# Kernel tuning notes

Measured on AMD Instinct MI355X. Metric: run time of the kernel, lower is better.

## Reference

```python
import jax, jax.numpy as jnp
import numpy as np

UNITS = 256
FEAT = 256
NUM_BLOCKS = 4  # start_gru + 2 middle blocks + end_gru
BATCH, T = 128, 384


def _gru_layer(x, kernel, rkernel, bias, return_sequences):
    """Keras GRU (reset_after=True, tanh/sigmoid), zero initial state.
    x: [B,T,D]; kernel: [D,3U]; rkernel: [U,3U]; bias: [2,3U] (input, recurrent).
    Gate order z, r, h as in Keras.
    """
    u = rkernel.shape[0]
    # Precompute input projections for all timesteps (one big GEMM)
    xp = jnp.einsum('btd,dg->btg', x, kernel) + bias[0]  # [B,T,3U]

    def step(h, xt):
        rh = h @ rkernel + bias[1]                 # [B,3U]
        mz, mr, mh = jnp.split(xt, 3, axis=-1)
        rz, rr, rhh = jnp.split(rh, 3, axis=-1)
        z = jax.nn.sigmoid(mz + rz)
        r = jax.nn.sigmoid(mr + rr)
        hh = jnp.tanh(mh + r * rhh)                # reset_after: r applied after recurrent matmul
        h_new = z * h + (1.0 - z) * hh
        return h_new, h_new

    h0 = jnp.zeros((x.shape[0], u), dtype=x.dtype)
    hT, hs = jax.lax.scan(step, h0, jnp.swapaxes(xp, 0, 1))  # scan over time
    return jnp.swapaxes(hs, 0, 1) if return_sequences else hT


def setup_inputs() -> dict:
    key = jax.random.key(0)
    ks = jax.random.split(key, 8)
    s_in = 1.0 / np.sqrt(FEAT)
    s_u = 1.0 / np.sqrt(UNITS)
    x = jax.random.normal(ks[0], (BATCH, T, FEAT), dtype=jnp.float32)
    # first layer params
    k0 = jax.random.normal(ks[1], (FEAT, 3 * UNITS), dtype=jnp.float32) * s_in
    rk0 = jax.random.normal(ks[2], (UNITS, 3 * UNITS), dtype=jnp.float32) * s_u
    b0 = jnp.zeros((2, 3 * UNITS), dtype=jnp.float32)
    # remaining NUM_BLOCKS-1 layers, stacked along leading axis
    L = NUM_BLOCKS - 1
    kern = jax.random.normal(ks[3], (L, UNITS, 3 * UNITS), dtype=jnp.float32) * s_u
    rkern = jax.random.normal(ks[4], (L, UNITS, 3 * UNITS), dtype=jnp.float32) * s_u
    bias = jnp.zeros((L, 2, 3 * UNITS), dtype=jnp.float32)
    return {"x": x, "k0": k0, "rk0": rk0, "b0": b0,
            "kern": kern, "rkern": rkern, "bias": bias}


def reference(x, k0, rk0, b0, kern, rkern, bias):
    # start_gru: return_sequences=True
    h = _gru_layer(x, k0, rk0, b0, return_sequences=True)
    L = kern.shape[0]
    # middle blocks return_sequences=True, last (end_gru) returns final state only
    for i in range(L):
        last = (i == L - 1)
        h = _gru_layer(h, kern[i], rkern[i], bias[i], return_sequences=not last)
    return h  # [B, UNITS]
```

## Files before the change

kernel.cpp:

```cpp
#include <hip/hip_runtime.h>
#include <hip/hip_fp16.h>


#define LAYERS 4
#define TSTEPS 384
#define NCH    8
#define WPL    (48 * 16 * 64 * 8)
#define TILE_STRIDE (16 * 64 * 8)
#define RING   16
#define SLOT_ULL (16 * 128)
#define GRP_ULL  (RING * SLOT_ULL)

typedef _Float16 half8 __attribute__((ext_vector_type(8)));
typedef float    f32x4 __attribute__((ext_vector_type(4)));
typedef unsigned uint4v __attribute__((ext_vector_type(4)));
typedef unsigned long long ull;

#define WP_OFF   0
#define BP_OFF   (LAYERS * WPL * 2)
#define FLAG_OFF (BP_OFF + LAYERS * 1024 * 4)
#define FLAG_BYTES 4096
#define HBUF_OFF (4 * 1024 * 1024)

#define SCOPE __HIP_MEMORY_SCOPE_AGENT
#define MFMA __builtin_amdgcn_mfma_f32_16x16x32_f16

__global__ void repack_kernel(const float* __restrict__ k0, const float* __restrict__ rk0,
                              const float* __restrict__ b0, const float* __restrict__ kern,
                              const float* __restrict__ rkern, const float* __restrict__ bias,
                              _Float16* __restrict__ Wp, float* __restrict__ Bp)
{
    int idx = blockIdx.x * 256 + threadIdx.x;
    const int total_w = LAYERS * WPL;
    if (idx < total_w) {
        int l = idx / WPL;
        int r = idx - l * WPL;
        int j    = r & 7;
        int lane = (r >> 3) & 63;
        int kt   = (r >> 9) & 15;
        int tile = r >> 13;
        int n = tile * 16 + (lane & 15);
        int k = kt * 32 + (lane >> 4) * 8 + j;
        float v;
        if (l == 0) {
            v = (k < 256) ? k0[(size_t)k * 768 + n] : rk0[(size_t)(k - 256) * 768 + n];
        } else {
            const float* kk = kern  + (size_t)(l - 1) * 256 * 768;
            const float* rk = rkern + (size_t)(l - 1) * 256 * 768;
            v = (k < 256) ? kk[(size_t)k * 768 + n] : rk[(size_t)(k - 256) * 768 + n];
        }
        Wp[idx] = (_Float16)v;
    } else {
        int ib = idx - total_w;
        if (ib < LAYERS * 1024) {
            int l = ib >> 10;
            int i = ib & 1023;
            const float* bs = (l == 0) ? b0 : (bias + (size_t)(l - 1) * 2 * 768);
            float v;
            if (i < 512)      v = bs[i] + bs[768 + i];
            else if (i < 768) v = bs[512 + (i - 512)];
            else              v = bs[768 + 512 + (i - 768)];
            Bp[l * 1024 + i] = v;
        }
    }
}

__launch_bounds__(512, 2)
__global__ void gru_kernel(const float* __restrict__ x,
                           const _Float16* __restrict__ Wp,
                           const float* __restrict__ Bp,
                           ull* __restrict__ hbuf,
                           unsigned int* __restrict__ flags,
                           float* __restrict__ out)
{
    __shared__ _Float16 Af[2][16 * 512];

    const int tid  = threadIdx.x;
    const int lane = tid & 63;
    const int w    = tid >> 6;
    const int lo16 = lane & 15;
    const int q    = lane >> 4;

    const int e = blockIdx.x & 1;
    const int c = (blockIdx.x >> 1) & 7;
    const int l = blockIdx.x >> 4;
    const int g = l * NCH + c;
    const int b0row = c * 16;

    half8 bzf[16], brf[16], bhf[16];
    {
        const _Float16* wb = Wp + (size_t)l * WPL;
        const int zt = 8 * e + w, rt = 16 + 8 * e + w, ht = 32 + 8 * e + w;
#pragma unroll
        for (int kt = 0; kt < 16; ++kt) {
            const size_t o = ((size_t)kt * 64 + lane) * 8;
            bzf[kt] = *(const half8*)(wb + (size_t)zt * TILE_STRIDE + o);
            brf[kt] = *(const half8*)(wb + (size_t)rt * TILE_STRIDE + o);
            bhf[kt] = *(const half8*)(wb + (size_t)ht * TILE_STRIDE + o);
        }
    }

    const int u0 = 128 * e + 16 * w + lo16;
    float Bz, Br, Bi, Bh;
    {
        const float* bp = Bp + l * 1024;
        Bz = bp[u0]; Br = bp[256 + u0]; Bi = bp[512 + u0]; Bh = bp[768 + u0];
    }

    const int grow = tid >> 4;
    const int g16  = tid & 15;
    const int gup  = g16 * 2;
    const int ktx  = g16 >> 1;
    const int qq   = (g16 & 1) * 2;
    const int xoff0 = ((ktx * 64) + qq * 16 + grow) * 8;
    const int xoff1 = ((ktx * 64) + (qq + 1) * 16 + grow) * 8;

    const int rr = tid >> 5;
    const int k5 = tid & 31;
    const int uown = 128 * e + 4 * k5;
    const int wown = 64 * e + 2 * k5;
    const int upar = 128 * (1 - e) + 4 * k5;
    const int wpar = 64 * (1 - e) + 2 * k5;
    auto hoff = [](int u, int r) {
        return ((8 + (u >> 5)) * 64 + ((u & 31) >> 3) * 16 + r) * 8 + (u & 7);
    };
    const int po = hoff(uown, rr);
    const int so = hoff(upar, rr);

    unsigned int* my_flag = flags + g * 2 + e;
    unsigned int* fl_dn   = flags + (g + NCH) * 2;

    ull*       hb_own = hbuf + (size_t)g * GRP_ULL;
    const ull* hb_up  = hbuf + (size_t)(l > 0 ? g - NCH : g) * GRP_ULL;

    auto wait_dn = [&](unsigned need) {
        for (;;) {
            unsigned v = 0xFFFFFFFFu;
            if (lane < 2)
                v = __hip_atomic_load(fl_dn + lane, __ATOMIC_RELAXED, SCOPE);
            if (__all((int)(v >= need))) return;
            __builtin_amdgcn_s_sleep(1);
        }
    };

    auto stage_x = [&](int t, _Float16* An) {
        if (l == 0) {
            const float* sp = x + ((size_t)(b0row + grow) * TSTEPS + t) * 256 + gup * 8;
            f32x4 a0 = *(const f32x4*)sp,       a1 = *(const f32x4*)(sp + 4);
            f32x4 a2 = *(const f32x4*)(sp + 8), a3 = *(const f32x4*)(sp + 12);
            half8 h0, h1;
            h0[0]=(_Float16)a0[0]; h0[1]=(_Float16)a0[1]; h0[2]=(_Float16)a0[2]; h0[3]=(_Float16)a0[3];
            h0[4]=(_Float16)a1[0]; h0[5]=(_Float16)a1[1]; h0[6]=(_Float16)a1[2]; h0[7]=(_Float16)a1[3];
            h1[0]=(_Float16)a2[0]; h1[1]=(_Float16)a2[1]; h1[2]=(_Float16)a2[2]; h1[3]=(_Float16)a2[3];
            h1[4]=(_Float16)a3[0]; h1[5]=(_Float16)a3[1]; h1[6]=(_Float16)a3[2]; h1[7]=(_Float16)a3[3];
            *(half8*)(An + xoff0) = h0;
            *(half8*)(An + xoff1) = h1;
        } else {
            const ull* spx = hb_up + (size_t)(t & (RING - 1)) * SLOT_ULL + grow * 128 + g16 * 8;
            const unsigned tg = (unsigned)(t + 1);
            ull vx[8];
#pragma unroll
            for (int j = 0; j < 8; ++j)
                vx[j] = __hip_atomic_load(spx + j, __ATOMIC_RELAXED, SCOPE);
            for (;;) {
                bool ok = true;
#pragma unroll
                for (int j = 0; j < 8; ++j)
                    if ((unsigned)(vx[j] >> 32) != tg) {
                        vx[j] = __hip_atomic_load(spx + j, __ATOMIC_RELAXED, SCOPE);
                        ok = false;
                    }
                if (ok) break;
                __builtin_amdgcn_s_sleep(1);
            }
            uint4v w0, w1;
            w0[0]=(unsigned)vx[0]; w0[1]=(unsigned)vx[1]; w0[2]=(unsigned)vx[2]; w0[3]=(unsigned)vx[3];
            w1[0]=(unsigned)vx[4]; w1[1]=(unsigned)vx[5]; w1[2]=(unsigned)vx[6]; w1[3]=(unsigned)vx[7];
            *(uint4v*)(An + xoff0) = w0;
            *(uint4v*)(An + xoff1) = w1;
        }
    };

    if (tid < 256) stage_x(0, Af[0]);
    {
        uint4v z = {0u, 0u, 0u, 0u};
        *(uint4v*)(Af[0] + ((8 + (tid >> 6)) * 64 + (tid & 63)) * 8) = z;
    }

    ull vh0, vh1;
    float hpv[4] = {0.f, 0.f, 0.f, 0.f};

    for (int t = 0; t < TSTEPS; ++t) {
        _Float16* A  = Af[t & 1];
        _Float16* An = Af[(t + 1) & 1];

        if (t > 0) {
            const ull* sp = hb_own + (size_t)((t - 1) & (RING - 1)) * SLOT_ULL + rr * 128 + wpar;
            const unsigned tg = (unsigned)t;
            for (;;) {
                bool ok = true;
                if ((unsigned)(vh0 >> 32) != tg) {
                    vh0 = __hip_atomic_load(sp + 0, __ATOMIC_RELAXED, SCOPE); ok = false;
                }
                if ((unsigned)(vh1 >> 32) != tg) {
                    vh1 = __hip_atomic_load(sp + 1, __ATOMIC_RELAXED, SCOPE); ok = false;
                }
                if (ok) break;
            }
            ull hv = ((ull)(unsigned)vh1 << 32) | (ull)(unsigned)vh0;
            *(ull*)(A + so) = hv;
        }
        __syncthreads();

        f32x4 az = {0,0,0,0}, ar = {0,0,0,0}, ai = {0,0,0,0}, ah = {0,0,0,0};
#pragma unroll
        for (int kt = 0; kt < 16; ++kt) {
            half8 a = *(const half8*)(A + ((kt * 64) + lane) * 8);
            az = MFMA(a, bzf[kt], az, 0, 0, 0);
            ar = MFMA(a, brf[kt], ar, 0, 0, 0);
            if (kt < 8) ai = MFMA(a, bhf[kt], ai, 0, 0, 0);
            else        ah = MFMA(a, bhf[kt], ah, 0, 0, 0);
        }

        float hn[4];
#pragma unroll
        for (int j = 0; j < 4; ++j) {
            float zp = az[j] + Bz;
            float rp = ar[j] + Br;
            float ip = ai[j] + Bi;
            float hp = ah[j] + Bh;
            float z  = 1.f / (1.f + __expf(-zp));
            float r  = 1.f / (1.f + __expf(-rp));
            float pre = ip + r * hp;
            float ex  = __expf(2.f * pre);
            float th  = 1.f - 2.f / (ex + 1.f);
            hn[j] = z * hpv[j] + (1.f - z) * th;
            hpv[j] = hn[j];
        }
#pragma unroll
        for (int j = 0; j < 4; ++j)
            An[hoff(u0, 4 * q + j)] = (_Float16)hn[j];
        if (l == 3 && t == TSTEPS - 1) {
#pragma unroll
            for (int j = 0; j < 4; ++j)
                out[(size_t)(b0row + 4 * q + j) * 256 + u0] = hn[j];
        }
        __syncthreads();

        if (l < 3 && t >= RING) wait_dn((unsigned)(t - RING + 1));

        {
            ull hv = *(const ull*)(An + po);
            ull* dst = hb_own + (size_t)(t & (RING - 1)) * SLOT_ULL + rr * 128 + wown;
            const ull tg = ((ull)(unsigned)(t + 1)) << 32;
            __hip_atomic_store(dst + 0, tg | (ull)(unsigned)hv,         __ATOMIC_RELAXED, SCOPE);
            __hip_atomic_store(dst + 1, tg | (ull)(unsigned)(hv >> 32), __ATOMIC_RELAXED, SCOPE);
        }

        if (t + 1 < TSTEPS) {
            if (tid < 256) stage_x(t + 1, An);
            const ull* sp = hb_own + (size_t)(t & (RING - 1)) * SLOT_ULL + rr * 128 + wpar;
            vh0 = __hip_atomic_load(sp + 0, __ATOMIC_RELAXED, SCOPE);
            vh1 = __hip_atomic_load(sp + 1, __ATOMIC_RELAXED, SCOPE);
        }
        __syncthreads();

        if (tid == 0)
            __hip_atomic_store(my_flag, (unsigned)(t + 1), __ATOMIC_RELAXED, SCOPE);
    }
}

extern "C" void kernel_launch(void* const* d_in, const int* in_sizes, int n_in,
                              void* d_out, int out_size, void* d_ws, size_t ws_size,
                              hipStream_t stream)
{
    const float* x     = (const float*)d_in[0];
    const float* k0    = (const float*)d_in[1];
    const float* rk0   = (const float*)d_in[2];
    const float* b0    = (const float*)d_in[3];
    const float* kern  = (const float*)d_in[4];
    const float* rkern = (const float*)d_in[5];
    const float* bias  = (const float*)d_in[6];
    float* out = (float*)d_out;

    char* ws = (char*)d_ws;
    _Float16*     Wp    = (_Float16*)(ws + WP_OFF);
    float*        Bp    = (float*)(ws + BP_OFF);
    unsigned int* flags = (unsigned int*)(ws + FLAG_OFF);
    ull*          hbuf  = (ull*)(ws + HBUF_OFF);

    hipMemsetAsync(flags, 0, FLAG_BYTES, stream);

    const int total = LAYERS * WPL + LAYERS * 1024;
    repack_kernel<<<(total + 255) / 256, 256, 0, stream>>>(k0, rk0, b0, kern, rkern, bias, Wp, Bp);

    gru_kernel<<<LAYERS * NCH * 2, 512, 0, stream>>>(x, Wp, Bp, hbuf, flags, out);
}
```

Baseline: 1.864 ms.

## Split fused GRU pipeline into per-segment input-projection and recurrence kernels

Replaces the single persistent wavefront-pipelined kernel, which ran all layers concurrently with flag and ring-buffer handoffs between blocks, by a host loop of 32 launches. Each layer and 96-step segment gets one input-projection kernel, a parallel GEMM over 32 blocks that writes precomputed gate inputs to global memory, followed by a recurrence kernel on 8 blocks. In the recurrence kernel each block holds all 256 units for 16 rows, so the cross-block hidden-state exchange disappears and only the recurrent matmul stays on the serial path. The cost is that layers now run one after another instead of overlapping, only 8 blocks do the serial work, and there is extra global traffic plus launch overhead.

```diff
diff --git a/kernel.cpp b/kernel.cpp
--- a/kernel.cpp
+++ b/kernel.cpp
@@ -1,15 +1,12 @@
 #include <hip/hip_runtime.h>
-#include <hip/hip_fp16.h>
 
 
 #define LAYERS 4
 #define TSTEPS 384
-#define NCH    8
+#define SEG    96
+#define NSEG   (TSTEPS / SEG)
 #define WPL    (48 * 16 * 64 * 8)
 #define TILE_STRIDE (16 * 64 * 8)
-#define RING   16
-#define SLOT_ULL (16 * 128)
-#define GRP_ULL  (RING * SLOT_ULL)
 
 typedef _Float16 half8 __attribute__((ext_vector_type(8)));
 typedef float    f32x4 __attribute__((ext_vector_type(4)));
@@ -17,12 +14,11 @@
 typedef unsigned long long ull;
 
 #define WP_OFF   0
-#define BP_OFF   (LAYERS * WPL * 2)
-#define FLAG_OFF (BP_OFF + LAYERS * 1024 * 4)
-#define FLAG_BYTES 4096
-#define HBUF_OFF (4 * 1024 * 1024)
-
-#define SCOPE __HIP_MEMORY_SCOPE_AGENT
+#define BP_OFF   3145728
+#define HST_OFF  3162112
+#define HSEQ_OFF 3407872
+#define XP_OFF   28573696
+
 #define MFMA __builtin_amdgcn_mfma_f32_16x16x32_f16
 
 __global__ void repack_kernel(const float* __restrict__ k0, const float* __restrict__ rk0,
@@ -66,208 +62,260 @@
 }
 
 __launch_bounds__(512, 2)
-__global__ void gru_kernel(const float* __restrict__ x,
-                           const _Float16* __restrict__ Wp,
-                           const float* __restrict__ Bp,
-                           ull* __restrict__ hbuf,
-                           unsigned int* __restrict__ flags,
-                           float* __restrict__ out)
+__global__ void xp_kernel(const float* __restrict__ x, const _Float16* __restrict__ Wp,
+                          const float* __restrict__ Bp, const _Float16* __restrict__ hseq,
+                          char* __restrict__ xp, int l, int t0seg)
 {
-    __shared__ _Float16 Af[2][16 * 512];
-
-    const int tid  = threadIdx.x;
-    const int lane = tid & 63;
-    const int w    = tid >> 6;
-    const int lo16 = lane & 15;
-    const int q    = lane >> 4;
-
-    const int e = blockIdx.x & 1;
-    const int c = (blockIdx.x >> 1) & 7;
-    const int l = blockIdx.x >> 4;
-    const int g = l * NCH + c;
+    __shared__ _Float16 Ax[2][4096];
+    __shared__ _Float16 Bl[16][4096];
+
+    const int tid = threadIdx.x, lane = tid & 63, w = tid >> 6;
+    const int lo16 = lane & 15, q = lane >> 4;
+    const int c = blockIdx.x & 7, tg = blockIdx.x >> 3;
+    const int nt = SEG / 4;
+    const int tb0 = t0seg + tg * nt;
     const int b0row = c * 16;
 
-    half8 bzf[16], brf[16], bhf[16];
+    half8 bz0f[8], bz1f[8], br0f[8], br1f[8];
     {
         const _Float16* wb = Wp + (size_t)l * WPL;
-        const int zt = 8 * e + w, rt = 16 + 8 * e + w, ht = 32 + 8 * e + w;
-#pragma unroll
-        for (int kt = 0; kt < 16; ++kt) {
+        const int zt0 = 2*w, zt1 = 2*w + 1, rt0 = 16 + 2*w, rt1 = 17 + 2*w;
+        const int it0 = 32 + 2*w, it1 = 33 + 2*w;
+#pragma unroll
+        for (int kt = 0; kt < 8; ++kt) {
             const size_t o = ((size_t)kt * 64 + lane) * 8;
-            bzf[kt] = *(const half8*)(wb + (size_t)zt * TILE_STRIDE + o);
-            brf[kt] = *(const half8*)(wb + (size_t)rt * TILE_STRIDE + o);
-            bhf[kt] = *(const half8*)(wb + (size_t)ht * TILE_STRIDE + o);
-        }
-    }
-
-    const int u0 = 128 * e + 16 * w + lo16;
-    float Bz, Br, Bi, Bh;
+            bz0f[kt] = *(const half8*)(wb + (size_t)zt0 * TILE_STRIDE + o);
+            bz1f[kt] = *(const half8*)(wb + (size_t)zt1 * TILE_STRIDE + o);
+            br0f[kt] = *(const half8*)(wb + (size_t)rt0 * TILE_STRIDE + o);
+            br1f[kt] = *(const half8*)(wb + (size_t)rt1 * TILE_STRIDE + o);
+            *(half8*)(&Bl[w*2+0][(kt*64+lane)*8]) = *(const half8*)(wb + (size_t)it0 * TILE_STRIDE + o);
+            *(half8*)(&Bl[w*2+1][(kt*64+lane)*8]) = *(const half8*)(wb + (size_t)it1 * TILE_STRIDE + o);
+        }
+    }
+    const int u0 = 32 * w + lo16, u1 = u0 + 16;
+    float bz0, bz1, br0, br1, bi0, bi1;
     {
         const float* bp = Bp + l * 1024;
-        Bz = bp[u0]; Br = bp[256 + u0]; Bi = bp[512 + u0]; Bh = bp[768 + u0];
-    }
-
-    const int grow = tid >> 4;
-    const int g16  = tid & 15;
-    const int gup  = g16 * 2;
-    const int ktx  = g16 >> 1;
-    const int qq   = (g16 & 1) * 2;
-    const int xoff0 = ((ktx * 64) + qq * 16 + grow) * 8;
-    const int xoff1 = ((ktx * 64) + (qq + 1) * 16 + grow) * 8;
-
-    const int rr = tid >> 5;
-    const int k5 = tid & 31;
-    const int uown = 128 * e + 4 * k5;
-    const int wown = 64 * e + 2 * k5;
-    const int upar = 128 * (1 - e) + 4 * k5;
-    const int wpar = 64 * (1 - e) + 2 * k5;
-    auto hoff = [](int u, int r) {
-        return ((8 + (u >> 5)) * 64 + ((u & 31) >> 3) * 16 + r) * 8 + (u & 7);
-    };
-    const int po = hoff(uown, rr);
-    const int so = hoff(upar, rr);
-
-    unsigned int* my_flag = flags + g * 2 + e;
-    unsigned int* fl_dn   = flags + (g + NCH) * 2;
-
-    ull*       hb_own = hbuf + (size_t)g * GRP_ULL;
-    const ull* hb_up  = hbuf + (size_t)(l > 0 ? g - NCH : g) * GRP_ULL;
-
-    auto wait_dn = [&](unsigned need) {
-        for (;;) {
-            unsigned v = 0xFFFFFFFFu;
-            if (lane < 2)
-                v = __hip_atomic_load(fl_dn + lane, __ATOMIC_RELAXED, SCOPE);
-            if (__all((int)(v >= need))) return;
-            __builtin_amdgcn_s_sleep(1);
-        }
-    };
-
-    auto stage_x = [&](int t, _Float16* An) {
-        if (l == 0) {
-            const float* sp = x + ((size_t)(b0row + grow) * TSTEPS + t) * 256 + gup * 8;
-            f32x4 a0 = *(const f32x4*)sp,       a1 = *(const f32x4*)(sp + 4);
-            f32x4 a2 = *(const f32x4*)(sp + 8), a3 = *(const f32x4*)(sp + 12);
-            half8 h0, h1;
-            h0[0]=(_Float16)a0[0]; h0[1]=(_Float16)a0[1]; h0[2]=(_Float16)a0[2]; h0[3]=(_Float16)a0[3];
-            h0[4]=(_Float16)a1[0]; h0[5]=(_Float16)a1[1]; h0[6]=(_Float16)a1[2]; h0[7]=(_Float16)a1[3];
-            h1[0]=(_Float16)a2[0]; h1[1]=(_Float16)a2[1]; h1[2]=(_Float16)a2[2]; h1[3]=(_Float16)a2[3];
-            h1[4]=(_Float16)a3[0]; h1[5]=(_Float16)a3[1]; h1[6]=(_Float16)a3[2]; h1[7]=(_Float16)a3[3];
-            *(half8*)(An + xoff0) = h0;
-            *(half8*)(An + xoff1) = h1;
-        } else {
-            const ull* spx = hb_up + (size_t)(t & (RING - 1)) * SLOT_ULL + grow * 128 + g16 * 8;
-            const unsigned tg = (unsigned)(t + 1);
-            ull vx[8];
-#pragma unroll
-            for (int j = 0; j < 8; ++j)
-                vx[j] = __hip_atomic_load(spx + j, __ATOMIC_RELAXED, SCOPE);
-            for (;;) {
-                bool ok = true;
-#pragma unroll
-                for (int j = 0; j < 8; ++j)
-                    if ((unsigned)(vx[j] >> 32) != tg) {
-                        vx[j] = __hip_atomic_load(spx + j, __ATOMIC_RELAXED, SCOPE);
-                        ok = false;
-                    }
-                if (ok) break;
-                __builtin_amdgcn_s_sleep(1);
+        bz0 = bp[u0];       bz1 = bp[u1];
+        br0 = bp[256 + u0]; br1 = bp[256 + u1];
+        bi0 = bp[512 + u0]; bi1 = bp[512 + u1];
+    }
+    const unsigned zo0 = (unsigned)(u0 * 32 + q * 8), zo1 = (unsigned)(u1 * 32 + q * 8);
+    const unsigned io0 = (unsigned)(16384 + u0 * 64 + q * 16);
+    const unsigned io1 = (unsigned)(16384 + u1 * 64 + q * 16);
+
+    if (l > 0) {
+        __syncthreads();
+        for (int i = 0; i < nt; ++i) {
+            const int t = tb0 + i;
+            const _Float16* hs = hseq + ((size_t)c * TSTEPS + t) * 4096;
+            f32x4 a0 = {bz0,bz0,bz0,bz0}, a1 = {bz1,bz1,bz1,bz1};
+            f32x4 a2 = {br0,br0,br0,br0}, a3 = {br1,br1,br1,br1};
+            f32x4 a4 = {bi0,bi0,bi0,bi0}, a5 = {bi1,bi1,bi1,bi1};
+#pragma unroll
+            for (int kt = 0; kt < 8; ++kt) {
+                half8 a  = *(const half8*)(hs + (kt * 64 + lane) * 8);
+                half8 b4 = *(const half8*)(&Bl[w*2+0][(kt*64+lane)*8]);
+                half8 b5 = *(const half8*)(&Bl[w*2+1][(kt*64+lane)*8]);
+                a0 = MFMA(a, bz0f[kt], a0, 0,0,0); a1 = MFMA(a, bz1f[kt], a1, 0,0,0);
+                a2 = MFMA(a, br0f[kt], a2, 0,0,0); a3 = MFMA(a, br1f[kt], a3, 0,0,0);
+                a4 = MFMA(a, b4, a4, 0,0,0);       a5 = MFMA(a, b5, a5, 0,0,0);
             }
-            uint4v w0, w1;
-            w0[0]=(unsigned)vx[0]; w0[1]=(unsigned)vx[1]; w0[2]=(unsigned)vx[2]; w0[3]=(unsigned)vx[3];
-            w1[0]=(unsigned)vx[4]; w1[1]=(unsigned)vx[5]; w1[2]=(unsigned)vx[6]; w1[3]=(unsigned)vx[7];
-            *(uint4v*)(An + xoff0) = w0;
-            *(uint4v*)(An + xoff1) = w1;
-        }
-    };
-
-    if (tid < 256) stage_x(0, Af[0]);
+            char* slot = xp + (size_t)(c * SEG + (t - t0seg)) * 32768;
+            union { ull u; _Float16 h[4]; } p;
+            p.h[0]=(_Float16)a0[0]; p.h[1]=(_Float16)a0[1]; p.h[2]=(_Float16)a0[2]; p.h[3]=(_Float16)a0[3];
+            *(ull*)(slot + zo0) = p.u;
+            p.h[0]=(_Float16)a1[0]; p.h[1]=(_Float16)a1[1]; p.h[2]=(_Float16)a1[2]; p.h[3]=(_Float16)a1[3];
+            *(ull*)(slot + zo1) = p.u;
+            p.h[0]=(_Float16)a2[0]; p.h[1]=(_Float16)a2[1]; p.h[2]=(_Float16)a2[2]; p.h[3]=(_Float16)a2[3];
+            *(ull*)(slot + 8192 + zo0) = p.u;
+            p.h[0]=(_Float16)a3[0]; p.h[1]=(_Float16)a3[1]; p.h[2]=(_Float16)a3[2]; p.h[3]=(_Float16)a3[3];
+            *(ull*)(slot + 8192 + zo1) = p.u;
+            *(f32x4*)(slot + io0) = a4;
+            *(f32x4*)(slot + io1) = a5;
+        }
+    } else {
+        const int row = tid >> 5, k8 = tid & 31;
+        auto stage = [&](int t, _Float16* A) {
+            const float* sp = x + ((size_t)(b0row + row) * TSTEPS + t) * 256 + k8 * 8;
+            f32x4 v0 = *(const f32x4*)sp, v1 = *(const f32x4*)(sp + 4);
+            half8 hh;
+            hh[0]=(_Float16)v0[0]; hh[1]=(_Float16)v0[1]; hh[2]=(_Float16)v0[2]; hh[3]=(_Float16)v0[3];
+            hh[4]=(_Float16)v1[0]; hh[5]=(_Float16)v1[1]; hh[6]=(_Float16)v1[2]; hh[7]=(_Float16)v1[3];
+            *(half8*)(A + ((k8 >> 2) * 64 + (k8 & 3) * 16 + row) * 8) = hh;
+        };
+        stage(tb0, Ax[0]);
+        for (int i = 0; i < nt; ++i) {
+            const int t = tb0 + i;
+            __syncthreads();
+            if (i + 1 < nt) stage(t + 1, Ax[(i + 1) & 1]);
+            const _Float16* A = Ax[i & 1];
+            f32x4 a0 = {bz0,bz0,bz0,bz0}, a1 = {bz1,bz1,bz1,bz1};
+            f32x4 a2 = {br0,br0,br0,br0}, a3 = {br1,br1,br1,br1};
+            f32x4 a4 = {bi0,bi0,bi0,bi0}, a5 = {bi1,bi1,bi1,bi1};
+#pragma unroll
+            for (int kt = 0; kt < 8; ++kt) {
+                half8 a  = *(const half8*)(A + (kt * 64 + lane) * 8);
+                half8 b4 = *(const half8*)(&Bl[w*2+0][(kt*64+lane)*8]);
+                half8 b5 = *(const half8*)(&Bl[w*2+1][(kt*64+lane)*8]);
+                a0 = MFMA(a, bz0f[kt], a0, 0,0,0); a1 = MFMA(a, bz1f[kt], a1, 0,0,0);
+                a2 = MFMA(a, br0f[kt], a2, 0,0,0); a3 = MFMA(a, br1f[kt], a3, 0,0,0);
+                a4 = MFMA(a, b4, a4, 0,0,0);       a5 = MFMA(a, b5, a5, 0,0,0);
+            }
+            char* slot = xp + (size_t)(c * SEG + (t - t0seg)) * 32768;
+            union { ull u; _Float16 h[4]; } p;
+            p.h[0]=(_Float16)a0[0]; p.h[1]=(_Float16)a0[1]; p.h[2]=(_Float16)a0[2]; p.h[3]=(_Float16)a0[3];
+            *(ull*)(slot + zo0) = p.u;
+            p.h[0]=(_Float16)a1[0]; p.h[1]=(_Float16)a1[1]; p.h[2]=(_Float16)a1[2]; p.h[3]=(_Float16)a1[3];
+            *(ull*)(slot + zo1) = p.u;
+            p.h[0]=(_Float16)a2[0]; p.h[1]=(_Float16)a2[1]; p.h[2]=(_Float16)a2[2]; p.h[3]=(_Float16)a2[3];
+            *(ull*)(slot + 8192 + zo0) = p.u;
+            p.h[0]=(_Float16)a3[0]; p.h[1]=(_Float16)a3[1]; p.h[2]=(_Float16)a3[2]; p.h[3]=(_Float16)a3[3];
+            *(ull*)(slot + 8192 + zo1) = p.u;
+            *(f32x4*)(slot + io0) = a4;
+            *(f32x4*)(slot + io1) = a5;
+        }
+    }
+}
+
+#define XPLOAD(i_, Z0, Z1, R0, R1, I0, I1) do {                                \
+    const char* s_ = xpc + (size_t)(i_) * 32768;                               \
+    Z0 = *(const ull*)(s_ + zo0);        Z1 = *(const ull*)(s_ + zo1);         \
+    R0 = *(const ull*)(s_ + 8192 + zo0); R1 = *(const ull*)(s_ + 8192 + zo1);  \
+    I0 = *(const f32x4*)(s_ + io0);      I1 = *(const f32x4*)(s_ + io1);       \
+} while (0)
+
+#define REC_BODY(IL, CUR, Z0, Z1, R0, R1, I0, I1, NZ0, NZ1, NR0, NR1, NI0, NI1) do { \
+    __syncthreads();                                                           \
+    if ((IL) + 1 < SEG) XPLOAD((IL) + 1, NZ0, NZ1, NR0, NR1, NI0, NI1);        \
+    const int T_ = t0seg + (IL);                                               \
+    if ((IL) > 0) {                                                            \
+        uint4v v_ = *(const uint4v*)(AhF + (CUR) * 4096 + tid * 8);            \
+        *(uint4v*)(hseqc + (size_t)(T_ - 1) * 8192 + tid * 16) = v_;           \
+    }                                                                          \
+    f32x4 az0 = {0,0,0,0}, az1 = {0,0,0,0}, ar0 = {0,0,0,0}, ar1 = {0,0,0,0};  \
+    f32x4 ah0 = {Bh0,Bh0,Bh0,Bh0}, ah1 = {Bh1,Bh1,Bh1,Bh1};                    \
+    _Pragma("unroll")                                                          \
+    for (int kt = 0; kt < 8; ++kt) {                                           \
+        half8 a  = *(const half8*)(AhF + (CUR) * 4096 + (kt * 64 + lane) * 8); \
+        half8 b4 = *(const half8*)(BlF + (w*2+0) * 4096 + (kt * 64 + lane) * 8); \
+        half8 b5 = *(const half8*)(BlF + (w*2+1) * 4096 + (kt * 64 + lane) * 8); \
+        az0 = MFMA(a, bz0f[kt], az0, 0,0,0); az1 = MFMA(a, bz1f[kt], az1, 0,0,0); \
+        ar0 = MFMA(a, br0f[kt], ar0, 0,0,0); ar1 = MFMA(a, br1f[kt], ar1, 0,0,0); \
+        ah0 = MFMA(a, b4, ah0, 0,0,0);       ah1 = MFMA(a, b5, ah1, 0,0,0);    \
+    }                                                                          \
+    union { ull u; _Float16 h[4]; } uz0_, uz1_, ur0_, ur1_;                    \
+    uz0_.u = Z0; uz1_.u = Z1; ur0_.u = R0; ur1_.u = R1;                        \
+    _Pragma("unroll")                                                          \
+    for (int j = 0; j < 4; ++j) {                                              \
+        float zp0 = az0[j] + (float)uz0_.h[j];                                 \
+        float rp0 = ar0[j] + (float)ur0_.h[j];                                 \
+        float z0 = 1.f / (1.f + __expf(-zp0));                                 \
+        float r0 = 1.f / (1.f + __expf(-rp0));                                 \
+        float pre0 = I0[j] + r0 * ah0[j];                                      \
+        float e0 = __expf(2.f * pre0);                                         \
+        float th0 = 1.f - 2.f / (e0 + 1.f);                                    \
+        float h0 = z0 * hp0[j] + (1.f - z0) * th0; hp0[j] = h0;                \
+        AhF[((CUR) ^ 1) * 4096 + ho0 + j * 8] = (_Float16)h0;                  \
+        float zp1 = az1[j] + (float)uz1_.h[j];                                 \
+        float rp1 = ar1[j] + (float)ur1_.h[j];                                 \
+        float z1 = 1.f / (1.f + __expf(-zp1));                                 \
+        float r1 = 1.f / (1.f + __expf(-rp1));                                 \
+        float pre1 = I1[j] + r1 * ah1[j];                                      \
+        float e1 = __expf(2.f * pre1);                                         \
+        float th1 = 1.f - 2.f / (e1 + 1.f);                                    \
+        float h1 = z1 * hp1[j] + (1.f - z1) * th1; hp1[j] = h1;                \
+        AhF[((CUR) ^ 1) * 4096 + ho1 + j * 8] = (_Float16)h1;                  \
+        if (isl3 && T_ == TSTEPS - 1) {                                        \
+            out[(size_t)(b0row + 4 * q + j) * 256 + u0] = h0;                  \
+            out[(size_t)(b0row + 4 * q + j) * 256 + u1] = h1;                  \
+        }                                                                      \
+    }                                                                          \
+} while (0)
+
+__launch_bounds__(512, 2)
+__global__ void rec_kernel(const _Float16* __restrict__ Wp, const float* __restrict__ Bp,
+                           _Float16* __restrict__ hseq, const char* __restrict__ xp,
+                           float* __restrict__ hst, float* __restrict__ out,
+                           int l, int t0seg)
+{
+    __shared__ _Float16 Ah[2][4096];
+    __shared__ _Float16 Bl[16][4096];
+    _Float16* AhF = &Ah[0][0];
+    _Float16* BlF = &Bl[0][0];
+
+    const int tid = threadIdx.x, lane = tid & 63, w = tid >> 6;
+    const int lo16 = lane & 15, q = lane >> 4;
+    const int c = blockIdx.x;
+    const int b0row = c * 16;
+    const bool isl3 = (l == 3);
+
+    half8 bz0f[8], bz1f[8], br0f[8], br1f[8];
     {
+        const _Float16* wb = Wp + (size_t)l * WPL;
+        const int zt0 = 2*w, zt1 = 2*w + 1, rt0 = 16 + 2*w, rt1 = 17 + 2*w;
+        const int it0 = 32 + 2*w, it1 = 33 + 2*w;
+#pragma unroll
+        for (int kt = 0; kt < 8; ++kt) {
+            const size_t o = ((size_t)(8 + kt) * 64 + lane) * 8;
+            bz0f[kt] = *(const half8*)(wb + (size_t)zt0 * TILE_STRIDE + o);
+            bz1f[kt] = *(const half8*)(wb + (size_t)zt1 * TILE_STRIDE + o);
+            br0f[kt] = *(const half8*)(wb + (size_t)rt0 * TILE_STRIDE + o);
+            br1f[kt] = *(const half8*)(wb + (size_t)rt1 * TILE_STRIDE + o);
+            *(half8*)(BlF + (w*2+0) * 4096 + (kt*64+lane)*8) = *(const half8*)(wb + (size_t)it0 * TILE_STRIDE + o);
+            *(half8*)(BlF + (w*2+1) * 4096 + (kt*64+lane)*8) = *(const half8*)(wb + (size_t)it1 * TILE_STRIDE + o);
+        }
+    }
+    const int u0 = 32 * w + lo16, u1 = u0 + 16;
+    const float Bh0 = Bp[l * 1024 + 768 + u0];
+    const float Bh1 = Bp[l * 1024 + 768 + u1];
+
+    const unsigned zo0 = (unsigned)(u0 * 32 + q * 8), zo1 = (unsigned)(u1 * 32 + q * 8);
+    const unsigned io0 = (unsigned)(16384 + u0 * 64 + q * 16);
+    const unsigned io1 = (unsigned)(16384 + u1 * 64 + q * 16);
+    const char* xpc = xp + (size_t)c * SEG * 32768;
+    char* hseqc = (char*)hseq + (size_t)c * TSTEPS * 8192;
+    char* hstc  = (char*)hst + (size_t)c * 16384;
+
+    const int ho0 = (w * 64 + (lo16 >> 3) * 16 + 4 * q) * 8 + (lo16 & 7);
+    const int ho1 = (w * 64 + (2 + (lo16 >> 3)) * 16 + 4 * q) * 8 + (lo16 & 7);
+
+    if (t0seg == 0) {
         uint4v z = {0u, 0u, 0u, 0u};
-        *(uint4v*)(Af[0] + ((8 + (tid >> 6)) * 64 + (tid & 63)) * 8) = z;
-    }
-
-    ull vh0, vh1;
-    float hpv[4] = {0.f, 0.f, 0.f, 0.f};
-
-    for (int t = 0; t < TSTEPS; ++t) {
-        _Float16* A  = Af[t & 1];
-        _Float16* An = Af[(t + 1) & 1];
-
-        if (t > 0) {
-            const ull* sp = hb_own + (size_t)((t - 1) & (RING - 1)) * SLOT_ULL + rr * 128 + wpar;
-            const unsigned tg = (unsigned)t;
-            for (;;) {
-                bool ok = true;
-                if ((unsigned)(vh0 >> 32) != tg) {
-                    vh0 = __hip_atomic_load(sp + 0, __ATOMIC_RELAXED, SCOPE); ok = false;
-                }
-                if ((unsigned)(vh1 >> 32) != tg) {
-                    vh1 = __hip_atomic_load(sp + 1, __ATOMIC_RELAXED, SCOPE); ok = false;
-                }
-                if (ok) break;
-            }
-            ull hv = ((ull)(unsigned)vh1 << 32) | (ull)(unsigned)vh0;
-            *(ull*)(A + so) = hv;
-        }
-        __syncthreads();
-
-        f32x4 az = {0,0,0,0}, ar = {0,0,0,0}, ai = {0,0,0,0}, ah = {0,0,0,0};
-#pragma unroll
-        for (int kt = 0; kt < 16; ++kt) {
-            half8 a = *(const half8*)(A + ((kt * 64) + lane) * 8);
-            az = MFMA(a, bzf[kt], az, 0, 0, 0);
-            ar = MFMA(a, brf[kt], ar, 0, 0, 0);
-            if (kt < 8) ai = MFMA(a, bhf[kt], ai, 0, 0, 0);
-            else        ah = MFMA(a, bhf[kt], ah, 0, 0, 0);
-        }
-
-        float hn[4];
-#pragma unroll
-        for (int j = 0; j < 4; ++j) {
-            float zp = az[j] + Bz;
-            float rp = ar[j] + Br;
-            float ip = ai[j] + Bi;
-            float hp = ah[j] + Bh;
-            float z  = 1.f / (1.f + __expf(-zp));
-            float r  = 1.f / (1.f + __expf(-rp));
-            float pre = ip + r * hp;
-            float ex  = __expf(2.f * pre);
-            float th  = 1.f - 2.f / (ex + 1.f);
-            hn[j] = z * hpv[j] + (1.f - z) * th;
-            hpv[j] = hn[j];
-        }
-#pragma unroll
-        for (int j = 0; j < 4; ++j)
-            An[hoff(u0, 4 * q + j)] = (_Float16)hn[j];
-        if (l == 3 && t == TSTEPS - 1) {
-#pragma unroll
-            for (int j = 0; j < 4; ++j)
-                out[(size_t)(b0row + 4 * q + j) * 256 + u0] = hn[j];
-        }
-        __syncthreads();
-
-        if (l < 3 && t >= RING) wait_dn((unsigned)(t - RING + 1));
-
-        {
-            ull hv = *(const ull*)(An + po);
-            ull* dst = hb_own + (size_t)(t & (RING - 1)) * SLOT_ULL + rr * 128 + wown;
-            const ull tg = ((ull)(unsigned)(t + 1)) << 32;
-            __hip_atomic_store(dst + 0, tg | (ull)(unsigned)hv,         __ATOMIC_RELAXED, SCOPE);
-            __hip_atomic_store(dst + 1, tg | (ull)(unsigned)(hv >> 32), __ATOMIC_RELAXED, SCOPE);
-        }
-
-        if (t + 1 < TSTEPS) {
-            if (tid < 256) stage_x(t + 1, An);
-            const ull* sp = hb_own + (size_t)(t & (RING - 1)) * SLOT_ULL + rr * 128 + wpar;
-            vh0 = __hip_atomic_load(sp + 0, __ATOMIC_RELAXED, SCOPE);
-            vh1 = __hip_atomic_load(sp + 1, __ATOMIC_RELAXED, SCOPE);
-        }
-        __syncthreads();
-
-        if (tid == 0)
-            __hip_atomic_store(my_flag, (unsigned)(t + 1), __ATOMIC_RELAXED, SCOPE);
-    }
+        *(uint4v*)(AhF + tid * 8) = z;
+    } else {
+        *(uint4v*)(AhF + tid * 8) =
+            *(const uint4v*)(hseqc + (size_t)(t0seg - 1) * 8192 + tid * 16);
+    }
+    float hp0[4], hp1[4];
+    if (t0seg == 0) {
+#pragma unroll
+        for (int j = 0; j < 4; ++j) { hp0[j] = 0.f; hp1[j] = 0.f; }
+    } else {
+        f32x4 v0 = *(const f32x4*)(hstc + u0 * 64 + q * 16);
+        f32x4 v1 = *(const f32x4*)(hstc + u1 * 64 + q * 16);
+#pragma unroll
+        for (int j = 0; j < 4; ++j) { hp0[j] = v0[j]; hp1[j] = v1[j]; }
+    }
+
+    ull zA0, zA1, rA0, rA1, zB0, zB1, rB0, rB1;
+    f32x4 iA0, iA1, iB0, iB1;
+    XPLOAD(0, zA0, zA1, rA0, rA1, iA0, iA1);
+
+    for (int i = 0; i < SEG; i += 2) {
+        REC_BODY(i,     0, zA0, zA1, rA0, rA1, iA0, iA1,
+                           zB0, zB1, rB0, rB1, iB0, iB1);
+        REC_BODY(i + 1, 1, zB0, zB1, rB0, rB1, iB0, iB1,
+                           zA0, zA1, rA0, rA1, iA0, iA1);
+    }
+
+    __syncthreads();
+    {
+        uint4v v = *(const uint4v*)(AhF + tid * 8);
+        *(uint4v*)(hseqc + (size_t)(t0seg + SEG - 1) * 8192 + tid * 16) = v;
+    }
+    *(f32x4*)(hstc + u0 * 64 + q * 16) = (f32x4){hp0[0], hp0[1], hp0[2], hp0[3]};
+    *(f32x4*)(hstc + u1 * 64 + q * 16) = (f32x4){hp1[0], hp1[1], hp1[2], hp1[3]};
 }
 
 extern "C" void kernel_launch(void* const* d_in, const int* in_sizes, int n_in,
@@ -284,15 +332,19 @@
     float* out = (float*)d_out;
 
     char* ws = (char*)d_ws;
-    _Float16*     Wp    = (_Float16*)(ws + WP_OFF);
-    float*        Bp    = (float*)(ws + BP_OFF);
-    unsigned int* flags = (unsigned int*)(ws + FLAG_OFF);
-    ull*          hbuf  = (ull*)(ws + HBUF_OFF);
-
-    hipMemsetAsync(flags, 0, FLAG_BYTES, stream);
+    _Float16* Wp   = (_Float16*)(ws + WP_OFF);
+    float*    Bp   = (float*)(ws + BP_OFF);
+    float*    hst  = (float*)(ws + HST_OFF);
+    _Float16* hseq = (_Float16*)(ws + HSEQ_OFF);
+    char*     xpb  = ws + XP_OFF;
 
     const int total = LAYERS * WPL + LAYERS * 1024;
     repack_kernel<<<(total + 255) / 256, 256, 0, stream>>>(k0, rk0, b0, kern, rkern, bias, Wp, Bp);
 
-    gru_kernel<<<LAYERS * NCH * 2, 512, 0, stream>>>(x, Wp, Bp, hbuf, flags, out);
+    for (int l = 0; l < LAYERS; ++l) {
+        for (int s = 0; s < NSEG; ++s) {
+            xp_kernel<<<32, 512, 0, stream>>>(x, Wp, Bp, hseq, xpb, l, s * SEG);
+            rec_kernel<<<8, 512, 0, stream>>>(Wp, Bp, hseq, xpb, hst, out, l, s * SEG);
+        }
+    }
 }
```

New measurement: 5.308 ms. +184.8%, slower.
